# Performance work log

Hardware: AMD Instinct MI355X
Metric: run time of the kernel (lower is better)

## Reference

```python
import jax, jax.numpy as jnp
import numpy as np


def setup_inputs() -> dict:
    key = jax.random.key(0)
    ks = jax.random.split(key, 8)
    B, C, H, W = 4, 256, 64, 64
    x = jax.random.normal(ks[0], (B, C, H, W), dtype=jnp.float32)
    y = jax.random.normal(ks[1], (B, C, H, W), dtype=jnp.float32)
    s = 1.0 / np.sqrt(C)
    Wq = jax.random.normal(ks[2], (C, C), dtype=jnp.float32) * s
    bq = jax.random.normal(ks[3], (C,), dtype=jnp.float32) * 0.02
    Wk = jax.random.normal(ks[4], (C, C), dtype=jnp.float32) * s
    bk = jax.random.normal(ks[5], (C,), dtype=jnp.float32) * 0.02
    Wv = jax.random.normal(ks[6], (C, C), dtype=jnp.float32) * s
    bv = jax.random.normal(ks[7], (C,), dtype=jnp.float32) * 0.02
    return {"x": x, "y": y, "Wq": Wq, "bq": bq, "Wk": Wk, "bk": bk, "Wv": Wv, "bv": bv}


def reference(x, y, Wq, bq, Wk, bk, Wv, bv):
    B, C, H, W = x.shape
    scale = C ** (-0.5)
    # flatten spatial dims: [B, N, C] with N = H*W
    x_flat = x.reshape(B, C, H * W).transpose(0, 2, 1)
    y_flat = y.reshape(B, C, H * W).transpose(0, 2, 1)
    # linear projections (torch Linear: x @ W.T + b)
    Q = jnp.einsum('bnc,dc->bnd', x_flat, Wq) + bq
    K = jnp.einsum('bnc,dc->bnd', y_flat, Wk) + bk
    V = jnp.einsum('bnc,dc->bnd', y_flat, Wv) + bv
    # single-head full cross-attention
    scores = jnp.einsum('bqd,bkd->bqk', Q, K) * scale  # [B, N, N]
    attn = jax.nn.softmax(scores, axis=-1)
    out = jnp.einsum('bqk,bkd->bqd', attn, V)  # [B, N, C]
    out = out.transpose(0, 2, 1).reshape(B, C, H, W)
    return x + out
```

## Files before the change

### kernel.cpp

```cpp
#include <hip/hip_runtime.h>
#include <stdint.h>

#define BN 4
#define CD 256
#define ND 4096
#define NK 32

typedef unsigned short u16;
typedef short bfrag __attribute__((ext_vector_type(8)));
typedef float ffrag __attribute__((ext_vector_type(4)));

__device__ __forceinline__ float bf2f(u16 u) {
  union { unsigned int i; float f; } v;
  v.i = ((unsigned int)u) << 16;
  return v.f;
}
__device__ __forceinline__ u16 f2bf(float f) {
  union { float f; unsigned int i; } v;
  v.f = f;
  return (u16)((v.i + 0x7FFFu + ((v.i >> 16) & 1u)) >> 16);
}
__device__ __forceinline__ void gload_lds(const u16* g, u16* l) {
  __builtin_amdgcn_global_load_lds(
      (const __attribute__((address_space(1))) void*)g,
      (__attribute__((address_space(3))) void*)l, 16, 0, 0);
}

__global__ __launch_bounds__(256, 2) void k_proj3(
    const float* __restrict__ x, const float* __restrict__ y,
    const float* __restrict__ Wq, const float* __restrict__ Wk,
    const float* __restrict__ Wv, const float* __restrict__ bq,
    const float* __restrict__ bk, const float* __restrict__ bv,
    u16* __restrict__ Qb, u16* __restrict__ Kb, u16* __restrict__ Vb) {
  __shared__ alignas(16) u16 S1[64][264];
  __shared__ alignas(16) u16 Ws[64][264];
  int t = threadIdx.x, w = t >> 6, l = t & 63;
  int lane16 = l & 15, quad = l >> 4;
  int zz = blockIdx.z;

  if (zz < 2) {
    int m0 = (blockIdx.y * 64 + blockIdx.x) * 64;
    int z = zz;
    int b = m0 >> 12, nsp = m0 & 4095;
    const float* src = (z ? y : x) + (size_t)b * CD * ND;
    const float* Wf = z ? Wk : Wq;
    const float* bias = z ? bk : bq;
    u16* Cd = (z ? Kb : Qb) + (size_t)m0 * CD;

    {
      int u = t & 15, grp = t >> 4;
#pragma unroll
      for (int it = 0; it < 16; ++it) {
        int c = it * 16 + grp;
        const float* col = src + (size_t)c * ND + nsp;
#pragma unroll
        for (int j = 0; j < 4; ++j)
          S1[j * 16 + u][c] = f2bf(col[j * 16 + u]);
      }
    }
    __syncthreads();

    bfrag af[8];
#pragma unroll
    for (int kc = 0; kc < 8; ++kc)
      af[kc] = *(const bfrag*)&S1[w * 16 + lane16][kc * 32 + quad * 8];

    ffrag acc[16];
#pragma unroll
    for (int i = 0; i < 16; ++i) acc[i] = ffrag{0.f, 0.f, 0.f, 0.f};

#pragma unroll
    for (int c4 = 0; c4 < 4; ++c4) {
      if (c4) __syncthreads();
#pragma unroll
      for (int it = 0; it < 16; ++it) {
        int idx = it * 256 + t;
        int row = idx >> 6, col = (idx & 63) * 4;
        float4 v = *(const float4*)(Wf + (size_t)(c4 * 64 + row) * CD + col);
        ushort4 o;
        o.x = f2bf(v.x); o.y = f2bf(v.y); o.z = f2bf(v.z); o.w = f2bf(v.w);
        *(ushort4*)&Ws[row][col] = o;
      }
      __syncthreads();
#pragma unroll
      for (int kc = 0; kc < 8; ++kc)
#pragma unroll
        for (int tt = 0; tt < 4; ++tt) {
          bfrag bfr = *(const bfrag*)&Ws[tt * 16 + lane16][kc * 32 + quad * 8];
          acc[c4 * 4 + tt] = __builtin_amdgcn_mfma_f32_16x16x32_bf16(
              af[kc], bfr, acc[c4 * 4 + tt], 0, 0, 0);
        }
    }
#pragma unroll
    for (int nt = 0; nt < 16; ++nt) {
      int col = nt * 16 + lane16;
      float bcol = bias[col];
#pragma unroll
      for (int r = 0; r < 4; ++r) {
        int rowL = w * 16 + quad * 4 + r;
        Cd[(size_t)rowL * CD + col] = f2bf(acc[nt][r] + bcol);
      }
    }
  } else {
    int n0s = blockIdx.x * 64;
    int b = blockIdx.y;
    const float* src = y + (size_t)b * CD * ND;
    u16* Cd = Vb + (size_t)b * CD * ND;

    {
      int u = t & 15, grp = t >> 4;
#pragma unroll
      for (int it = 0; it < 16; ++it) {
        int c = it * 16 + grp;
        const float* col = src + (size_t)c * ND + n0s;
#pragma unroll
        for (int j = 0; j < 4; ++j)
          S1[j * 16 + u][c] = f2bf(col[j * 16 + u]);
      }
    }
    __syncthreads();

    bfrag bfr8[8];
#pragma unroll
    for (int kc = 0; kc < 8; ++kc)
      bfr8[kc] = *(const bfrag*)&S1[w * 16 + lane16][kc * 32 + quad * 8];

    ffrag o[16];
#pragma unroll
    for (int i = 0; i < 16; ++i) o[i] = ffrag{0.f, 0.f, 0.f, 0.f};

#pragma unroll
    for (int c4 = 0; c4 < 4; ++c4) {
      if (c4) __syncthreads();
#pragma unroll
      for (int it = 0; it < 16; ++it) {
        int idx = it * 256 + t;
        int row = idx >> 6, col = (idx & 63) * 4;
        float4 v = *(const float4*)(Wv + (size_t)(c4 * 64 + row) * CD + col);
        ushort4 ov;
        ov.x = f2bf(v.x); ov.y = f2bf(v.y); ov.z = f2bf(v.z); ov.w = f2bf(v.w);
        *(ushort4*)&Ws[row][col] = ov;
      }
      __syncthreads();
#pragma unroll
      for (int kc = 0; kc < 8; ++kc)
#pragma unroll
        for (int mt = 0; mt < 4; ++mt) {
          bfrag af = *(const bfrag*)&Ws[mt * 16 + lane16][kc * 32 + quad * 8];
          o[c4 * 4 + mt] = __builtin_amdgcn_mfma_f32_16x16x32_bf16(
              af, bfr8[kc], o[c4 * 4 + mt], 0, 0, 0);
        }
    }
#pragma unroll
    for (int i = 0; i < 16; ++i) {
      int c4 = i >> 2, mt = i & 3;
#pragma unroll
      for (int r = 0; r < 4; ++r) {
        int d = c4 * 64 + mt * 16 + quad * 4 + r;
        Cd[(size_t)d * ND + n0s + w * 16 + lane16] = f2bf(o[i][r] + bv[d]);
      }
    }
  }
}

union SmemU {
  struct {
    u16 Ks[2][NK][256];
    u16 Vs[2][CD][NK];
    u16 Ps[8][16][40];
  } a;
  u16 ot[CD][136];
};

template <int NS>
__global__ __launch_bounds__(256, 2) void k_attn(
    const u16* __restrict__ Q, const u16* __restrict__ K,
    const u16* __restrict__ Vt, u16* __restrict__ O01,
    u16* __restrict__ O23, float* __restrict__ Lpart) {
  constexpr int NIT = ND / NS / NK;
  __shared__ alignas(16) SmemU sm;
  int b = blockIdx.y, q0 = blockIdx.x * 128, z = blockIdx.z;
  int t = threadIdx.x, w = t >> 6, l = t & 63;
  int lane16 = l & 15, quad = l >> 4;
  const float scale = 0.0625f;

  bfrag qf[2][8];
#pragma unroll
  for (int mi = 0; mi < 2; ++mi) {
    const u16* Qrow =
        Q + ((size_t)b * ND + q0 + (w * 2 + mi) * 16 + lane16) * CD;
#pragma unroll
    for (int kc = 0; kc < 8; ++kc)
      qf[mi][kc] = *(const bfrag*)(Qrow + kc * 32 + quad * 8);
  }

  ffrag o[2][16];
#pragma unroll
  for (int mi = 0; mi < 2; ++mi)
#pragma unroll
    for (int i = 0; i < 16; ++i) o[mi][i] = ffrag{0.f, 0.f, 0.f, 0.f};
  float lsum[2][4] = {{0.f, 0.f, 0.f, 0.f}, {0.f, 0.f, 0.f, 0.f}};

  const u16* Kb = K + ((size_t)b * ND + z * (ND / NS)) * CD;
  const u16* Vb = Vt + (size_t)b * CD * ND + z * (ND / NS);

  auto stage = [&](int kt2) {
    int dbuf = kt2 & 1;
    const u16* Kt = Kb + (size_t)kt2 * NK * CD;
    const u16* Vtt = Vb + kt2 * NK;
#pragma unroll
    for (int p = 0; p < 4; ++p) {
      int r = p * 8 + w * 2 + (l >> 5);
      int j = (l & 31) ^ (r & 7);
      gload_lds(Kt + (size_t)r * CD + j * 8, &sm.a.Ks[dbuf][p * 8 + w * 2][0]);
    }
#pragma unroll
    for (int p = 0; p < 4; ++p) {
      int dd = p * 64 + w * 16 + (l >> 2);
      int j = (l & 3) ^ ((dd >> 1) & 3);
      gload_lds(Vtt + (size_t)dd * ND + j * 8, &sm.a.Vs[dbuf][p * 64 + w * 16][0]);
    }
  };

  stage(0);
  for (int kt = 0; kt < NIT; ++kt) {
    int dbuf = kt & 1;
    __syncthreads();
    if (kt + 1 < NIT) stage(kt + 1);

    ffrag s2[2][2];
#pragma unroll
    for (int mi = 0; mi < 2; ++mi)
#pragma unroll
      for (int tt = 0; tt < 2; ++tt) s2[mi][tt] = ffrag{0.f, 0.f, 0.f, 0.f};
#pragma unroll
    for (int kc = 0; kc < 8; ++kc) {
      bfrag kf0, kf1;
      {
        int r = lane16;
        int cp = (kc * 4 + quad) ^ (r & 7);
        kf0 = *(const bfrag*)&sm.a.Ks[dbuf][r][cp * 8];
        int r1 = 16 + lane16;
        int cp1 = (kc * 4 + quad) ^ (r1 & 7);
        kf1 = *(const bfrag*)&sm.a.Ks[dbuf][r1][cp1 * 8];
      }
#pragma unroll
      for (int mi = 0; mi < 2; ++mi) {
        s2[mi][0] = __builtin_amdgcn_mfma_f32_16x16x32_bf16(qf[mi][kc], kf0,
                                                            s2[mi][0], 0, 0, 0);
        s2[mi][1] = __builtin_amdgcn_mfma_f32_16x16x32_bf16(qf[mi][kc], kf1,
                                                            s2[mi][1], 0, 0, 0);
      }
    }

#pragma unroll
    for (int mi = 0; mi < 2; ++mi)
#pragma unroll
      for (int tt = 0; tt < 2; ++tt)
#pragma unroll
        for (int r = 0; r < 4; ++r) {
          float p = __expf(s2[mi][tt][r] * scale);
          lsum[mi][r] += p;
          sm.a.Ps[w * 2 + mi][quad * 4 + r][tt * 16 + lane16] = f2bf(p);
        }
    bfrag pf0 = *(const bfrag*)&sm.a.Ps[w * 2 + 0][lane16][quad * 8];
    bfrag pf1 = *(const bfrag*)&sm.a.Ps[w * 2 + 1][lane16][quad * 8];

#pragma unroll
    for (int dt = 0; dt < 16; ++dt) {
      int dd = dt * 16 + lane16;
      int cp = quad ^ ((dd >> 1) & 3);
      bfrag vf = *(const bfrag*)&sm.a.Vs[dbuf][dd][cp * 8];
      o[0][dt] = __builtin_amdgcn_mfma_f32_16x16x32_bf16(pf0, vf, o[0][dt], 0, 0, 0);
      o[1][dt] = __builtin_amdgcn_mfma_f32_16x16x32_bf16(pf1, vf, o[1][dt], 0, 0, 0);
    }
  }

#pragma unroll
  for (int mi = 0; mi < 2; ++mi)
#pragma unroll
    for (int r = 0; r < 4; ++r) {
#pragma unroll
      for (int off = 1; off < 16; off <<= 1)
        lsum[mi][r] += __shfl_xor(lsum[mi][r], off, 64);
    }
  if (lane16 == 0) {
#pragma unroll
    for (int mi = 0; mi < 2; ++mi)
#pragma unroll
      for (int r = 0; r < 4; ++r)
        Lpart[((size_t)z * BN + b) * ND + q0 + (w * 2 + mi) * 16 + quad * 4 + r] =
            lsum[mi][r];
  }

  __syncthreads();
#pragma unroll
  for (int mi = 0; mi < 2; ++mi)
#pragma unroll
    for (int dt = 0; dt < 16; ++dt)
#pragma unroll
      for (int r = 0; r < 4; ++r)
        sm.ot[dt * 16 + lane16][(w * 2 + mi) * 16 + quad * 4 + r] =
            f2bf(o[mi][dt][r]);
  __syncthreads();
  const size_t SZc = (size_t)BN * ND * CD;
  u16* Op = ((z < 2) ? O01 : O23) + (size_t)(z & 1) * SZc;
#pragma unroll
  for (int it = 0; it < 16; ++it) {
    int c = it * 256 + t;
    int dd = c >> 4, co = (c & 15) * 8;
    size_t g = ((size_t)b * CD + dd) * ND + q0 + co;
    *(uint4*)(Op + g) = *(const uint4*)&sm.ot[dd][co];
  }
}

template <int NS>
__global__ __launch_bounds__(256) void k_combine(
    const u16* __restrict__ O01, const u16* __restrict__ O23,
    const float* __restrict__ L, const float* __restrict__ x,
    float* __restrict__ out) {
  const size_t SZc = (size_t)BN * ND * CD;
  size_t e = ((size_t)blockIdx.x * 256 + threadIdx.x) * 8;
  int n = (int)(e & (ND - 1));
  int b = (int)(e >> 20);
  float ls[8] = {0, 0, 0, 0, 0, 0, 0, 0};
  float acc[8] = {0, 0, 0, 0, 0, 0, 0, 0};
#pragma unroll
  for (int z = 0; z < NS; ++z) {
    const float* Lr = L + ((size_t)z * BN + b) * ND + n;
    float4 l0 = *(const float4*)(Lr);
    float4 l1 = *(const float4*)(Lr + 4);
    ls[0] += l0.x; ls[1] += l0.y; ls[2] += l0.z; ls[3] += l0.w;
    ls[4] += l1.x; ls[5] += l1.y; ls[6] += l1.z; ls[7] += l1.w;
    const u16* Oz = ((z < 2) ? O01 : O23) + (size_t)(z & 1) * SZc + e;
    union { uint4 q; u16 s[8]; } u;
    u.q = *(const uint4*)Oz;
#pragma unroll
    for (int j = 0; j < 8; ++j) acc[j] += bf2f(u.s[j]);
  }
  float4 x0 = *(const float4*)(x + e);
  float4 x1 = *(const float4*)(x + e + 4);
  float4 r0, r1;
  r0.x = x0.x + acc[0] / ls[0];
  r0.y = x0.y + acc[1] / ls[1];
  r0.z = x0.z + acc[2] / ls[2];
  r0.w = x0.w + acc[3] / ls[3];
  r1.x = x1.x + acc[4] / ls[4];
  r1.y = x1.y + acc[5] / ls[5];
  r1.z = x1.z + acc[6] / ls[6];
  r1.w = x1.w + acc[7] / ls[7];
  *(float4*)(out + e) = r0;
  *(float4*)(out + e + 4) = r1;
}

extern "C" void kernel_launch(void* const* d_in, const int* in_sizes, int n_in,
                              void* d_out, int out_size, void* d_ws, size_t ws_size,
                              hipStream_t stream) {
  const float* x  = (const float*)d_in[0];
  const float* y  = (const float*)d_in[1];
  const float* Wq = (const float*)d_in[2];
  const float* bq = (const float*)d_in[3];
  const float* Wk = (const float*)d_in[4];
  const float* bk = (const float*)d_in[5];
  const float* Wv = (const float*)d_in[6];
  const float* bv = (const float*)d_in[7];
  float* out = (float*)d_out;
  u16* ws = (u16*)d_ws;
  const size_t SZ = (size_t)BN * ND * CD;
  u16* Qb = ws;
  u16* Kb = Qb + SZ;
  u16* Vb = Kb + SZ;
  u16* Ob = Vb + SZ;
  const size_t need4 = 7 * SZ * sizeof(u16) + (size_t)4 * BN * ND * sizeof(float);
  const bool big = ws_size >= need4;
  const int cgrid = (int)(SZ / (256 * 8));

  k_proj3<<<dim3(64, 4, 3), 256, 0, stream>>>(x, y, Wq, Wk, Wv, bq, bk, bv,
                                              Qb, Kb, Vb);
  if (big) {
    float* Lp = (float*)(Ob + 4 * SZ);
    k_attn<4><<<dim3(ND / 128, BN, 4), 256, 0, stream>>>(Qb, Kb, Vb, Ob,
                                                         Ob + 2 * SZ, Lp);
    k_combine<4><<<dim3(cgrid), 256, 0, stream>>>(Ob, Ob + 2 * SZ, Lp, x, out);
  } else {
    float* Lp = (float*)(Ob + 2 * SZ);
    k_attn<2><<<dim3(ND / 128, BN, 2), 256, 0, stream>>>(Qb, Kb, Vb, Ob, Ob, Lp);
    k_combine<2><<<dim3(cgrid), 256, 0, stream>>>(Ob, Ob, Lp, x, out);
  }
}
```

Measured before the change: 194.5 us.

## Prepack projection weights into MFMA fragment layout with a separate kernel

Adds a small kernel that converts Wq/Wk/Wv to bf16 once per call and stores them in the exact per-lane MFMA fragment order. The projection kernel then reads B/A fragments straight from global memory (L2-resident) instead of repeatedly converting fp32 weights into a shared-memory tile with barriers. This drops the Ws shared buffer and raises the occupancy hint from 2 to 4 blocks per CU. The cost is an extra launch and workspace space for the packed weights.

```diff
diff --git a/kernel.cpp b/kernel.cpp
--- a/kernel.cpp
+++ b/kernel.cpp
@@ -5,6 +5,7 @@
 #define CD 256
 #define ND 4096
 #define NK 32
+#define WPK_M 65536
 
 typedef unsigned short u16;
 typedef short bfrag __attribute__((ext_vector_type(8)));
@@ -26,26 +27,42 @@
       (__attribute__((address_space(3))) void*)l, 16, 0, 0);
 }
 
-__global__ __launch_bounds__(256, 2) void k_proj3(
+__global__ __launch_bounds__(256) void k_packW(
+    const float* __restrict__ Wq, const float* __restrict__ Wk,
+    const float* __restrict__ Wv, u16* __restrict__ Wpk) {
+  int idx = blockIdx.x * 256 + threadIdx.x;
+  int lane = idx & 63;
+  int fb = idx >> 6;
+  int nt = fb & 15, kc = (fb >> 4) & 7, m = fb >> 7;
+  const float* W = (m == 0) ? Wq : ((m == 1) ? Wk : Wv);
+  const float* s = W + (size_t)(nt * 16 + (lane & 15)) * CD + kc * 32 + (lane >> 4) * 8;
+  u16* d = Wpk + (size_t)m * WPK_M + ((size_t)(kc * 16 + nt)) * 512 + lane * 8;
+  float4 v0 = *(const float4*)(s);
+  float4 v1 = *(const float4*)(s + 4);
+  ushort4 o0, o1;
+  o0.x = f2bf(v0.x); o0.y = f2bf(v0.y); o0.z = f2bf(v0.z); o0.w = f2bf(v0.w);
+  o1.x = f2bf(v1.x); o1.y = f2bf(v1.y); o1.z = f2bf(v1.z); o1.w = f2bf(v1.w);
+  *(ushort4*)(d) = o0;
+  *(ushort4*)(d + 4) = o1;
+}
+
+__global__ __launch_bounds__(256, 4) void k_proj3(
     const float* __restrict__ x, const float* __restrict__ y,
-    const float* __restrict__ Wq, const float* __restrict__ Wk,
-    const float* __restrict__ Wv, const float* __restrict__ bq,
+    const u16* __restrict__ Wpk, const float* __restrict__ bq,
     const float* __restrict__ bk, const float* __restrict__ bv,
     u16* __restrict__ Qb, u16* __restrict__ Kb, u16* __restrict__ Vb) {
   __shared__ alignas(16) u16 S1[64][264];
-  __shared__ alignas(16) u16 Ws[64][264];
   int t = threadIdx.x, w = t >> 6, l = t & 63;
   int lane16 = l & 15, quad = l >> 4;
   int zz = blockIdx.z;
 
   if (zz < 2) {
     int m0 = (blockIdx.y * 64 + blockIdx.x) * 64;
-    int z = zz;
     int b = m0 >> 12, nsp = m0 & 4095;
-    const float* src = (z ? y : x) + (size_t)b * CD * ND;
-    const float* Wf = z ? Wk : Wq;
-    const float* bias = z ? bk : bq;
-    u16* Cd = (z ? Kb : Qb) + (size_t)m0 * CD;
+    const float* src = (zz ? y : x) + (size_t)b * CD * ND;
+    const float* bias = zz ? bk : bq;
+    u16* Cd = (zz ? Kb : Qb) + (size_t)m0 * CD;
+    const u16* Wz = Wpk + (size_t)zz * WPK_M;
 
     {
       int u = t & 15, grp = t >> 4;
@@ -70,26 +87,13 @@
     for (int i = 0; i < 16; ++i) acc[i] = ffrag{0.f, 0.f, 0.f, 0.f};
 
 #pragma unroll
-    for (int c4 = 0; c4 < 4; ++c4) {
-      if (c4) __syncthreads();
-#pragma unroll
-      for (int it = 0; it < 16; ++it) {
-        int idx = it * 256 + t;
-        int row = idx >> 6, col = (idx & 63) * 4;
-        float4 v = *(const float4*)(Wf + (size_t)(c4 * 64 + row) * CD + col);
-        ushort4 o;
-        o.x = f2bf(v.x); o.y = f2bf(v.y); o.z = f2bf(v.z); o.w = f2bf(v.w);
-        *(ushort4*)&Ws[row][col] = o;
-      }
-      __syncthreads();
-#pragma unroll
-      for (int kc = 0; kc < 8; ++kc)
-#pragma unroll
-        for (int tt = 0; tt < 4; ++tt) {
-          bfrag bfr = *(const bfrag*)&Ws[tt * 16 + lane16][kc * 32 + quad * 8];
-          acc[c4 * 4 + tt] = __builtin_amdgcn_mfma_f32_16x16x32_bf16(
-              af[kc], bfr, acc[c4 * 4 + tt], 0, 0, 0);
-        }
+    for (int kc = 0; kc < 8; ++kc) {
+      const u16* base = Wz + ((size_t)kc * 16) * 512 + l * 8;
+#pragma unroll
+      for (int nt = 0; nt < 16; ++nt) {
+        bfrag bfr = *(const bfrag*)(base + nt * 512);
+        acc[nt] = __builtin_amdgcn_mfma_f32_16x16x32_bf16(af[kc], bfr, acc[nt], 0, 0, 0);
+      }
     }
 #pragma unroll
     for (int nt = 0; nt < 16; ++nt) {
@@ -106,6 +110,7 @@
     int b = blockIdx.y;
     const float* src = y + (size_t)b * CD * ND;
     u16* Cd = Vb + (size_t)b * CD * ND;
+    const u16* Wz = Wpk + (size_t)2 * WPK_M;
 
     {
       int u = t & 15, grp = t >> 4;
@@ -130,34 +135,20 @@
     for (int i = 0; i < 16; ++i) o[i] = ffrag{0.f, 0.f, 0.f, 0.f};
 
 #pragma unroll
-    for (int c4 = 0; c4 < 4; ++c4) {
-      if (c4) __syncthreads();
-#pragma unroll
-      for (int it = 0; it < 16; ++it) {
-        int idx = it * 256 + t;
-        int row = idx >> 6, col = (idx & 63) * 4;
-        float4 v = *(const float4*)(Wv + (size_t)(c4 * 64 + row) * CD + col);
-        ushort4 ov;
-        ov.x = f2bf(v.x); ov.y = f2bf(v.y); ov.z = f2bf(v.z); ov.w = f2bf(v.w);
-        *(ushort4*)&Ws[row][col] = ov;
-      }
-      __syncthreads();
-#pragma unroll
-      for (int kc = 0; kc < 8; ++kc)
-#pragma unroll
-        for (int mt = 0; mt < 4; ++mt) {
-          bfrag af = *(const bfrag*)&Ws[mt * 16 + lane16][kc * 32 + quad * 8];
-          o[c4 * 4 + mt] = __builtin_amdgcn_mfma_f32_16x16x32_bf16(
-              af, bfr8[kc], o[c4 * 4 + mt], 0, 0, 0);
-        }
-    }
-#pragma unroll
-    for (int i = 0; i < 16; ++i) {
-      int c4 = i >> 2, mt = i & 3;
+    for (int kc = 0; kc < 8; ++kc) {
+      const u16* base = Wz + ((size_t)kc * 16) * 512 + l * 8;
+#pragma unroll
+      for (int mt = 0; mt < 16; ++mt) {
+        bfrag af = *(const bfrag*)(base + mt * 512);
+        o[mt] = __builtin_amdgcn_mfma_f32_16x16x32_bf16(af, bfr8[kc], o[mt], 0, 0, 0);
+      }
+    }
+#pragma unroll
+    for (int mt = 0; mt < 16; ++mt) {
 #pragma unroll
       for (int r = 0; r < 4; ++r) {
-        int d = c4 * 64 + mt * 16 + quad * 4 + r;
-        Cd[(size_t)d * ND + n0s + w * 16 + lane16] = f2bf(o[i][r] + bv[d]);
+        int d = mt * 16 + quad * 4 + r;
+        Cd[(size_t)d * ND + n0s + w * 16 + lane16] = f2bf(o[mt][r] + bv[d]);
       }
     }
   }
@@ -371,19 +362,27 @@
   u16* Kb = Qb + SZ;
   u16* Vb = Kb + SZ;
   u16* Ob = Vb + SZ;
-  const size_t need4 = 7 * SZ * sizeof(u16) + (size_t)4 * BN * ND * sizeof(float);
+  const size_t need4 = 7 * SZ * sizeof(u16) +
+                       (size_t)4 * BN * ND * sizeof(float) +
+                       (size_t)3 * WPK_M * sizeof(u16);
   const bool big = ws_size >= need4;
   const int cgrid = (int)(SZ / (256 * 8));
 
-  k_proj3<<<dim3(64, 4, 3), 256, 0, stream>>>(x, y, Wq, Wk, Wv, bq, bk, bv,
-                                              Qb, Kb, Vb);
   if (big) {
     float* Lp = (float*)(Ob + 4 * SZ);
+    u16* Wpk = (u16*)(Lp + (size_t)4 * BN * ND);
+    k_packW<<<dim3(96), 256, 0, stream>>>(Wq, Wk, Wv, Wpk);
+    k_proj3<<<dim3(64, 4, 3), 256, 0, stream>>>(x, y, Wpk, bq, bk, bv,
+                                                Qb, Kb, Vb);
     k_attn<4><<<dim3(ND / 128, BN, 4), 256, 0, stream>>>(Qb, Kb, Vb, Ob,
                                                          Ob + 2 * SZ, Lp);
     k_combine<4><<<dim3(cgrid), 256, 0, stream>>>(Ob, Ob + 2 * SZ, Lp, x, out);
   } else {
     float* Lp = (float*)(Ob + 2 * SZ);
+    u16* Wpk = (u16*)(Lp + (size_t)2 * BN * ND);
+    k_packW<<<dim3(96), 256, 0, stream>>>(Wq, Wk, Wv, Wpk);
+    k_proj3<<<dim3(64, 4, 3), 256, 0, stream>>>(x, y, Wpk, bq, bk, bv,
+                                                Qb, Kb, Vb);
     k_attn<2><<<dim3(ND / 128, BN, 2), 256, 0, stream>>>(Qb, Kb, Vb, Ob, Ob, Lp);
     k_combine<2><<<dim3(cgrid), 256, 0, stream>>>(Ob, Ob, Lp, x, out);
   }
```

After: 193.3 us. About the same (-0.7%).
